# Kernel optimization log

Measured on AMD Instinct MI355X. Metric: run time of the kernel, lower is better.

## Reference

```python
import jax, jax.numpy as jnp
import numpy as np

N_NODES = 50000
N_EDGES = 800000
IN_CH = 64
HID = 64
HID2 = HID // 2  # 32


def _sage_conv(x, src, dst, w_l, w_r, b, n_nodes):
    """PyG SAGEConv (aggr='mean', root_weight=True):
    out = lin_l(mean_{j in N(i)} x_j) + lin_r(x_i), bias in lin_l.
    Messages flow src -> dst (source_to_target)."""
    msg = x[src]  # [E, d] gather of source features
    summed = jax.ops.segment_sum(msg, dst, num_segments=n_nodes)  # [N, d]
    cnt = jax.ops.segment_sum(jnp.ones((src.shape[0],), x.dtype), dst,
                              num_segments=n_nodes)  # [N]
    mean = summed / jnp.maximum(cnt, 1.0)[:, None]
    return mean @ w_l + b + x @ w_r


def setup_inputs() -> dict:
    key = jax.random.key(0)
    ks = jax.random.split(key, 12)
    s = 0.05
    x = jax.random.normal(ks[0], (N_NODES, IN_CH), dtype=jnp.float32)
    edge_index = jax.random.randint(ks[1], (2, N_EDGES), 0, N_NODES, dtype=jnp.int32)
    return {
        "x": x,
        "edge_index": edge_index,
        # SAGEConv layer 1 (in -> hidden)
        "w1_l": jax.random.normal(ks[2], (IN_CH, HID), dtype=jnp.float32) * s,
        "w1_r": jax.random.normal(ks[3], (IN_CH, HID), dtype=jnp.float32) * s,
        "b1": jnp.zeros((HID,), jnp.float32),
        # SAGEConv layer 2 (hidden -> hidden//2)
        "w2_l": jax.random.normal(ks[4], (HID, HID2), dtype=jnp.float32) * s,
        "w2_r": jax.random.normal(ks[5], (HID, HID2), dtype=jnp.float32) * s,
        "b2": jnp.zeros((HID2,), jnp.float32),
        # classifier MLP: Linear(32,16) -> ReLU -> Linear(16,2)
        "wc1": jax.random.normal(ks[6], (HID2, 16), dtype=jnp.float32) * s,
        "bc1": jnp.zeros((16,), jnp.float32),
        "wc2": jax.random.normal(ks[7], (16, 2), dtype=jnp.float32) * s,
        "bc2": jnp.zeros((2,), jnp.float32),
    }


def reference(x, edge_index, w1_l, w1_r, b1, w2_l, w2_r, b2, wc1, bc1, wc2, bc2):
    src, dst = edge_index[0], edge_index[1]
    n = x.shape[0]
    # Dropout is identity in eval / deterministic reference.
    h = jax.nn.relu(_sage_conv(x, src, dst, w1_l, w1_r, b1, n))
    h = jax.nn.relu(_sage_conv(h, src, dst, w2_l, w2_r, b2, n))
    h = jax.nn.relu(h @ wc1 + bc1)
    out = h @ wc2 + bc2  # [N, 2]
    return out
```

## Files before the change

kernel.cpp:

```cpp
#include <hip/hip_runtime.h>
#include <hip/hip_fp16.h>

#define N_NODES 50000
#define N_EDGES 800000
#define NBINS   391
#define CAP     4096
#define EPB     4096
#define NBLK_E  ((N_EDGES + EPB - 1) / EPB)
#define NTILE   391
#define LSTRIDE 129

__global__ __launch_bounds__(512) void k_binA_pre1(
        const int* __restrict__ src, const int* __restrict__ dst,
        int* __restrict__ bincur, int* __restrict__ binned,
        const float* __restrict__ x,
        const float* __restrict__ wl, const float* __restrict__ wr,
        const float* __restrict__ b,
        __half* __restrict__ ph, float* __restrict__ q) {
    __shared__ float smem[64 * LSTRIDE];
    int t = threadIdx.x;
    int bb = blockIdx.x;
    if (bb < NBLK_E) {
        int* cnt  = (int*)smem;
        int* sc   = cnt + 392;
        int* lpos = sc + 512;
        int* base = lpos + 392;
        int* stage = base + 392;
        unsigned short* sbin = (unsigned short*)(stage + EPB);
        int blkbase = bb * EPB;
        int nE = min(EPB, N_EDGES - blkbase);
        for (int i = t; i < NBINS; i += 512) cnt[i] = 0;
        __syncthreads();
        int sv[8], dv[8];
#pragma unroll
        for (int k = 0; k < 8; ++k) {
            int e = blkbase + t + k * 512;
            if (e < N_EDGES) {
                sv[k] = src[e];
                dv[k] = dst[e];
                atomicAdd(&cnt[dv[k] >> 7], 1);
            } else dv[k] = -1;
        }
        __syncthreads();
        sc[t] = (t < NBINS) ? cnt[t] : 0;
        __syncthreads();
        for (int d = 1; d < 512; d <<= 1) {
            int add = (t >= d) ? sc[t - d] : 0;
            __syncthreads();
            sc[t] += add;
            __syncthreads();
        }
        for (int bi = t; bi < NBINS; bi += 512) {
            int excl = sc[bi] - cnt[bi];
            lpos[bi] = excl;
            sc[bi] = excl;
            if (cnt[bi] > 0) base[bi] = bi * CAP + atomicAdd(&bincur[bi], cnt[bi]);
        }
        __syncthreads();
#pragma unroll
        for (int k = 0; k < 8; ++k) {
            if (dv[k] >= 0) {
                int bi = dv[k] >> 7;
                int p = atomicAdd(&lpos[bi], 1);
                stage[p] = (sv[k] & 0xFFFF) | ((dv[k] & 127) << 16);
                sbin[p] = (unsigned short)bi;
            }
        }
        __syncthreads();
        for (int i = t; i < nE; i += 512) {
            int bi = sbin[i];
            int pos = base[bi] + (i - sc[bi]);
            if (pos < (bi + 1) * CAP) binned[pos] = stage[i];
        }
        return;
    }
    float* sx = smem;
    int g0 = (bb - NBLK_E) * 128;
#pragma unroll
    for (int i = 0; i < 4; ++i) {
        int f = t + i * 512;
        int nd = f >> 4, cq = f & 15;
        int gn = g0 + nd;
        float4 v = (gn < N_NODES) ? ((const float4*)x)[(size_t)gn * 16 + cq]
                                  : make_float4(0.f, 0.f, 0.f, 0.f);
        sx[(cq * 4 + 0) * LSTRIDE + nd] = v.x;
        sx[(cq * 4 + 1) * LSTRIDE + nd] = v.y;
        sx[(cq * 4 + 2) * LSTRIDE + nd] = v.z;
        sx[(cq * 4 + 3) * LSTRIDE + nd] = v.w;
    }
    __syncthreads();
    int role = __builtin_amdgcn_readfirstlane(t >> 7);
    int wsel = role >> 1;
    int c0 = (role & 1) * 32;
    int ln = t & 127;
    int node = g0 + ln;
    const float* __restrict__ wm = wsel ? wr : wl;
    float acc[32];
    if (wsel) {
#pragma unroll
        for (int c = 0; c < 32; ++c) acc[c] = b[c0 + c];
    } else {
#pragma unroll
        for (int c = 0; c < 32; ++c) acc[c] = 0.f;
    }
#pragma unroll
    for (int k = 0; k < 64; ++k) {
        float xk = sx[k * LSTRIDE + ln];
#pragma unroll
        for (int c = 0; c < 32; ++c)
            acc[c] = fmaf(xk, wm[k * 64 + c0 + c], acc[c]);
    }
    if (node >= N_NODES) return;
    if (wsel == 0) {
        alignas(16) __half2 hv[16];
#pragma unroll
        for (int i = 0; i < 16; ++i)
            hv[i] = __floats2half2_rn(acc[2 * i], acc[2 * i + 1]);
        float4* op = (float4*)(ph + (size_t)node * 64 + c0);
#pragma unroll
        for (int i = 0; i < 4; ++i) op[i] = ((float4*)hv)[i];
    } else {
        float4* op = (float4*)(q + (size_t)node * 64 + c0);
#pragma unroll
        for (int i = 0; i < 8; ++i)
            op[i] = make_float4(acc[4 * i], acc[4 * i + 1], acc[4 * i + 2], acc[4 * i + 3]);
    }
}

__device__ __forceinline__ void add8(float2& c0, float2& c1, float2& c2, float2& c3,
                                     float4 rv) {
    const __half2* hp = (const __half2*)&rv;
    float2 f0 = __half22float2(hp[0]), f1 = __half22float2(hp[1]);
    float2 f2 = __half22float2(hp[2]), f3 = __half22float2(hp[3]);
    c0.x += f0.x; c0.y += f0.y; c1.x += f1.x; c1.y += f1.y;
    c2.x += f2.x; c2.y += f2.y; c3.x += f3.x; c3.y += f3.y;
}

#define RED2(v, M0, M1)                                         \
    v.x += __shfl_xor(v.x, M0); v.y += __shfl_xor(v.y, M0);     \
    v.x += __shfl_xor(v.x, M1); v.y += __shfl_xor(v.y, M1);

__global__ __launch_bounds__(1024) void k_sort_agg1_pre2(
        const int* __restrict__ bincur, const int* __restrict__ binned,
        int* __restrict__ off, unsigned short* __restrict__ deg,
        int* __restrict__ esrc,
        const __half* __restrict__ ph, const float* __restrict__ q,
        const float* __restrict__ w2l, const float* __restrict__ w2r,
        const float* __restrict__ b2,
        __half* __restrict__ zh, float* __restrict__ r) {
    __shared__ float poolA[64 * LSTRIDE];
    __shared__ int   sbuf[CAP];
    __shared__ int   loff[128];
    __shared__ int   ldeg[128];
    int t = threadIdx.x;
    int bb = blockIdx.x;
    int n0 = bb << 7;
    int seg0 = bb * CAP;
    int n = min(bincur[bb], CAP);
    int* wbuf = (int*)poolA;
    int* cnt  = wbuf + CAP;
    int* tmp  = cnt + 128;
    int* cur  = tmp + 128;
    if (t < 128) cnt[t] = 0;
    for (int i = t; i < n; i += 1024) wbuf[i] = binned[seg0 + i];
    __syncthreads();
    for (int i = t; i < n; i += 1024) atomicAdd(&cnt[wbuf[i] >> 16], 1);
    __syncthreads();
    int v = (t < 128) ? cnt[t] : 0;
    if (t < 128) tmp[t] = v;
    __syncthreads();
    int val = v;
    for (int d = 1; d < 128; d <<= 1) {
        int add = (t >= d && t < 128) ? tmp[t - d] : 0;
        __syncthreads();
        if (t < 128) { val += add; tmp[t] = val; }
        __syncthreads();
    }
    if (t < 128) {
        int excl = val - v;
        cur[t] = excl;
        loff[t] = excl;
        ldeg[t] = v;
        int node = n0 + t;
        if (node < N_NODES) {
            off[node] = seg0 + excl;
            deg[node] = (unsigned short)v;
        }
    }
    __syncthreads();
    for (int i = t; i < n; i += 1024) {
        int w = wbuf[i];
        int p = atomicAdd(&cur[w >> 16], 1);
        sbuf[p] = w & 0xFFFF;
    }
    __syncthreads();
    for (int i = t; i < n; i += 1024) esrc[seg0 + i] = sbuf[i];
    float* sx = poolA;
    {
        int grp = t >> 3;
        int cg  = t & 7;
        int node = n0 + grp;
        if (node < N_NODES) {
            int s0 = loff[grp];
            int dv = ldeg[grp];
            int s1 = s0 + dv;
            const __half* __restrict__ phc = ph + (cg << 3);
            float2 A0 = make_float2(0.f, 0.f), A1 = A0, A2 = A0, A3 = A0;
            float2 B0 = A0, B1 = A0, B2 = A0, B3 = A0;
            float2 C0 = A0, C1 = A0, C2 = A0, C3 = A0;
            float2 D0 = A0, D1 = A0, D2 = A0, D3 = A0;
            for (int i = s0; i < s1; i += 4) {
                add8(A0, A1, A2, A3,
                     *(const float4*)(phc + (size_t)sbuf[i] * 64));
                if (i + 1 < s1) add8(B0, B1, B2, B3,
                     *(const float4*)(phc + (size_t)sbuf[i + 1] * 64));
                if (i + 2 < s1) add8(C0, C1, C2, C3,
                     *(const float4*)(phc + (size_t)sbuf[i + 2] * 64));
                if (i + 3 < s1) add8(D0, D1, D2, D3,
                     *(const float4*)(phc + (size_t)sbuf[i + 3] * 64));
            }
            A0.x += B0.x + (C0.x + D0.x); A0.y += B0.y + (C0.y + D0.y);
            A1.x += B1.x + (C1.x + D1.x); A1.y += B1.y + (C1.y + D1.y);
            A2.x += B2.x + (C2.x + D2.x); A2.y += B2.y + (C2.y + D2.y);
            A3.x += B3.x + (C3.x + D3.x); A3.y += B3.y + (C3.y + D3.y);
            float inv = 1.0f / fmaxf((float)dv, 1.0f);
            const float4* qp = (const float4*)(q + (size_t)node * 64 + (cg << 3));
            float4 q0 = qp[0], q1 = qp[1];
            float* d = sx + (cg << 3) * LSTRIDE + grp;
            d[0 * LSTRIDE] = fmaxf(fmaf(A0.x, inv, q0.x), 0.f);
            d[1 * LSTRIDE] = fmaxf(fmaf(A0.y, inv, q0.y), 0.f);
            d[2 * LSTRIDE] = fmaxf(fmaf(A1.x, inv, q0.z), 0.f);
            d[3 * LSTRIDE] = fmaxf(fmaf(A1.y, inv, q0.w), 0.f);
            d[4 * LSTRIDE] = fmaxf(fmaf(A2.x, inv, q1.x), 0.f);
            d[5 * LSTRIDE] = fmaxf(fmaf(A2.y, inv, q1.y), 0.f);
            d[6 * LSTRIDE] = fmaxf(fmaf(A3.x, inv, q1.z), 0.f);
            d[7 * LSTRIDE] = fmaxf(fmaf(A3.y, inv, q1.w), 0.f);
        }
    }
    __syncthreads();
    int g = __builtin_amdgcn_readfirstlane(t >> 7);
    int role = g & 1;
    int c0 = (g >> 1) * 8;
    int ln = t & 127;
    int node = n0 + ln;
    const float* __restrict__ wm = role ? w2r : w2l;
    float acc[8];
    if (role) {
#pragma unroll
        for (int c = 0; c < 8; ++c) acc[c] = b2[c0 + c];
    } else {
#pragma unroll
        for (int c = 0; c < 8; ++c) acc[c] = 0.f;
    }
#pragma unroll
    for (int k = 0; k < 64; ++k) {
        float xk = sx[k * LSTRIDE + ln];
#pragma unroll
        for (int c = 0; c < 8; ++c)
            acc[c] = fmaf(xk, wm[k * 32 + c0 + c], acc[c]);
    }
    if (node >= N_NODES) return;
    if (role == 0) {
        alignas(16) __half2 hv[4];
#pragma unroll
        for (int i = 0; i < 4; ++i)
            hv[i] = __floats2half2_rn(acc[2 * i], acc[2 * i + 1]);
        *(float4*)(zh + (size_t)node * 32 + c0) = *(float4*)hv;
    } else {
        float4* op = (float4*)(r + (size_t)node * 32 + c0);
        op[0] = make_float4(acc[0], acc[1], acc[2], acc[3]);
        op[1] = make_float4(acc[4], acc[5], acc[6], acc[7]);
    }
}

__global__ __launch_bounds__(256) void k_agg2cls(const int* __restrict__ off,
                                                 const unsigned short* __restrict__ deg,
                                                 const int* __restrict__ esrc,
                                                 const __half* __restrict__ zh,
                                                 const float* __restrict__ r,
                                                 const float* __restrict__ wc1,
                                                 const float* __restrict__ bc1,
                                                 const float* __restrict__ wc2,
                                                 const float* __restrict__ bc2,
                                                 float* __restrict__ out) {
    __shared__ float sh2[16 * 33];
    __shared__ float sh3[16 * 17];
    __shared__ float swc1[512];
    __shared__ float sbc1[16];
    __shared__ float swc2[32];
    __shared__ float sbc2[2];
    int t = threadIdx.x;
    swc1[t] = wc1[t];
    swc1[t + 256] = wc1[t + 256];
    if (t < 16) sbc1[t] = bc1[t];
    if (t < 32) swc2[t] = wc2[t];
    if (t < 2)  sbc2[t] = bc2[t];

    int lane = t & 63;
    int l16 = lane & 15;
    int nl = (t >> 4) & 15;
    int node = blockIdx.x * 16 + nl;
    int eg = l16 >> 2;
    int cg = l16 & 3;
    int s0 = off[node];
    int dv = deg[node];
    int s1 = s0 + dv;
    float2 A0 = make_float2(0.f, 0.f), A1 = A0, A2 = A0, A3 = A0;
    float2 B0 = A0, B1 = A0, B2 = A0, B3 = A0;
    for (int i = s0; i < s1; i += 8) {
        int i0 = i + eg, i1 = i + 4 + eg;
        if (i0 < s1) add8(A0, A1, A2, A3,
            *(const float4*)(zh + (size_t)esrc[i0] * 32 + (cg << 3)));
        if (i1 < s1) add8(B0, B1, B2, B3,
            *(const float4*)(zh + (size_t)esrc[i1] * 32 + (cg << 3)));
    }
    A0.x += B0.x; A0.y += B0.y; A1.x += B1.x; A1.y += B1.y;
    A2.x += B2.x; A2.y += B2.y; A3.x += B3.x; A3.y += B3.y;
    RED2(A0, 4, 8); RED2(A1, 4, 8); RED2(A2, 4, 8); RED2(A3, 4, 8);
    if (eg == 0) {
        float inv = 1.0f / fmaxf((float)dv, 1.0f);
        const float4* rp = (const float4*)(r + (size_t)node * 32 + (cg << 3));
        float4 r0 = rp[0], r1 = rp[1];
        float* d = sh2 + nl * 33 + (cg << 3);
        d[0] = fmaxf(fmaf(A0.x, inv, r0.x), 0.f);
        d[1] = fmaxf(fmaf(A0.y, inv, r0.y), 0.f);
        d[2] = fmaxf(fmaf(A1.x, inv, r0.z), 0.f);
        d[3] = fmaxf(fmaf(A1.y, inv, r0.w), 0.f);
        d[4] = fmaxf(fmaf(A2.x, inv, r1.x), 0.f);
        d[5] = fmaxf(fmaf(A2.y, inv, r1.y), 0.f);
        d[6] = fmaxf(fmaf(A3.x, inv, r1.z), 0.f);
        d[7] = fmaxf(fmaf(A3.y, inv, r1.w), 0.f);
    }
    __syncthreads();
    int n = t >> 4, j = t & 15;
    float acc1 = sbc1[j];
#pragma unroll
    for (int k = 0; k < 32; ++k)
        acc1 = fmaf(sh2[n * 33 + k], swc1[k * 16 + j], acc1);
    sh3[n * 17 + j] = fmaxf(acc1, 0.f);
    __syncthreads();
    if (t < 16) {
        int nn = t;
        float o0 = sbc2[0], o1 = sbc2[1];
#pragma unroll
        for (int k = 0; k < 16; ++k) {
            float h3k = sh3[nn * 17 + k];
            o0 = fmaf(h3k, swc2[k * 2 + 0], o0);
            o1 = fmaf(h3k, swc2[k * 2 + 1], o1);
        }
        int gnode = blockIdx.x * 16 + nn;
        *(float2*)(out + (size_t)gnode * 2) = make_float2(o0, o1);
    }
}

extern "C" void kernel_launch(void* const* d_in, const int* in_sizes, int n_in,
                              void* d_out, int out_size, void* d_ws, size_t ws_size,
                              hipStream_t stream) {
    const float* x   = (const float*)d_in[0];
    const int*   ei  = (const int*)d_in[1];
    const int*   src = ei;
    const int*   dst = ei + N_EDGES;
    const float* w1l = (const float*)d_in[2];
    const float* w1r = (const float*)d_in[3];
    const float* b1  = (const float*)d_in[4];
    const float* w2l = (const float*)d_in[5];
    const float* w2r = (const float*)d_in[6];
    const float* b2  = (const float*)d_in[7];
    const float* wc1 = (const float*)d_in[8];
    const float* bc1 = (const float*)d_in[9];
    const float* wc2 = (const float*)d_in[10];
    const float* bc2 = (const float*)d_in[11];
    float* out = (float*)d_out;

    int*   wi     = (int*)d_ws;
    int*   bincur = wi;
    int*   binned = wi + 400;
    int*   esrc   = binned + (size_t)NBINS * CAP;
    int*   off    = esrc + (size_t)NBINS * CAP;
    unsigned short* deg = (unsigned short*)(off + N_NODES);
    float* q      = (float*)(deg + N_NODES + (N_NODES & 1));
    float* phf    = q + (size_t)64 * N_NODES;
    __half* ph    = (__half*)phf;
    float* zhf    = phf + (size_t)32 * N_NODES;
    __half* zh    = (__half*)zhf;
    float* r      = zhf + (size_t)16 * N_NODES;

    hipMemsetAsync(bincur, 0, 400 * sizeof(int), stream);
    k_binA_pre1<<<NBLK_E + NTILE, 512, 0, stream>>>(src, dst, bincur, binned,
                                                    x, w1l, w1r, b1, ph, q);
    k_sort_agg1_pre2<<<NBINS, 1024, 0, stream>>>(bincur, binned, off, deg, esrc,
                                                 ph, q, w2l, w2r, b2, zh, r);
    k_agg2cls<<<N_NODES / 16, 256, 0, stream>>>(off, deg, esrc, zh, r,
                                                wc1, bc1, wc2, bc2, out);
}
```

Before: 165.8 us.

## Remap layer-2 aggregation to 4 threads per node, 64 nodes per block

```diff
diff --git a/kernel.cpp b/kernel.cpp
--- a/kernel.cpp
+++ b/kernel.cpp
@@ -135,10 +135,6 @@
     c0.x += f0.x; c0.y += f0.y; c1.x += f1.x; c1.y += f1.y;
     c2.x += f2.x; c2.y += f2.y; c3.x += f3.x; c3.y += f3.y;
 }
-
-#define RED2(v, M0, M1)                                         \
-    v.x += __shfl_xor(v.x, M0); v.y += __shfl_xor(v.y, M0);     \
-    v.x += __shfl_xor(v.x, M1); v.y += __shfl_xor(v.y, M1);
 
 __global__ __launch_bounds__(1024) void k_sort_agg1_pre2(
         const int* __restrict__ bincur, const int* __restrict__ binned,
@@ -283,8 +279,8 @@
                                                  const float* __restrict__ wc2,
                                                  const float* __restrict__ bc2,
                                                  float* __restrict__ out) {
-    __shared__ float sh2[16 * 33];
-    __shared__ float sh3[16 * 17];
+    __shared__ float sh2[64 * 33];
+    __shared__ float sh3[64 * 17];
     __shared__ float swc1[512];
     __shared__ float sbc1[16];
     __shared__ float swc2[32];
@@ -295,61 +291,76 @@
     if (t < 16) sbc1[t] = bc1[t];
     if (t < 32) swc2[t] = wc2[t];
     if (t < 2)  sbc2[t] = bc2[t];
-
-    int lane = t & 63;
-    int l16 = lane & 15;
-    int nl = (t >> 4) & 15;
-    int node = blockIdx.x * 16 + nl;
-    int eg = l16 >> 2;
-    int cg = l16 & 3;
-    int s0 = off[node];
-    int dv = deg[node];
-    int s1 = s0 + dv;
-    float2 A0 = make_float2(0.f, 0.f), A1 = A0, A2 = A0, A3 = A0;
-    float2 B0 = A0, B1 = A0, B2 = A0, B3 = A0;
-    for (int i = s0; i < s1; i += 8) {
-        int i0 = i + eg, i1 = i + 4 + eg;
-        if (i0 < s1) add8(A0, A1, A2, A3,
-            *(const float4*)(zh + (size_t)esrc[i0] * 32 + (cg << 3)));
-        if (i1 < s1) add8(B0, B1, B2, B3,
-            *(const float4*)(zh + (size_t)esrc[i1] * 32 + (cg << 3)));
-    }
-    A0.x += B0.x; A0.y += B0.y; A1.x += B1.x; A1.y += B1.y;
-    A2.x += B2.x; A2.y += B2.y; A3.x += B3.x; A3.y += B3.y;
-    RED2(A0, 4, 8); RED2(A1, 4, 8); RED2(A2, 4, 8); RED2(A3, 4, 8);
-    if (eg == 0) {
-        float inv = 1.0f / fmaxf((float)dv, 1.0f);
-        const float4* rp = (const float4*)(r + (size_t)node * 32 + (cg << 3));
-        float4 r0 = rp[0], r1 = rp[1];
-        float* d = sh2 + nl * 33 + (cg << 3);
-        d[0] = fmaxf(fmaf(A0.x, inv, r0.x), 0.f);
-        d[1] = fmaxf(fmaf(A0.y, inv, r0.y), 0.f);
-        d[2] = fmaxf(fmaf(A1.x, inv, r0.z), 0.f);
-        d[3] = fmaxf(fmaf(A1.y, inv, r0.w), 0.f);
-        d[4] = fmaxf(fmaf(A2.x, inv, r1.x), 0.f);
-        d[5] = fmaxf(fmaf(A2.y, inv, r1.y), 0.f);
-        d[6] = fmaxf(fmaf(A3.x, inv, r1.z), 0.f);
-        d[7] = fmaxf(fmaf(A3.y, inv, r1.w), 0.f);
-    }
-    __syncthreads();
-    int n = t >> 4, j = t & 15;
-    float acc1 = sbc1[j];
-#pragma unroll
-    for (int k = 0; k < 32; ++k)
-        acc1 = fmaf(sh2[n * 33 + k], swc1[k * 16 + j], acc1);
-    sh3[n * 17 + j] = fmaxf(acc1, 0.f);
-    __syncthreads();
-    if (t < 16) {
-        int nn = t;
-        float o0 = sbc2[0], o1 = sbc2[1];
-#pragma unroll
-        for (int k = 0; k < 16; ++k) {
-            float h3k = sh3[nn * 17 + k];
-            o0 = fmaf(h3k, swc2[k * 2 + 0], o0);
-            o1 = fmaf(h3k, swc2[k * 2 + 1], o1);
-        }
-        int gnode = blockIdx.x * 16 + nn;
-        *(float2*)(out + (size_t)gnode * 2) = make_float2(o0, o1);
+    __syncthreads();
+
+    int n0 = blockIdx.x << 6;
+    {
+        int nd = t >> 2;
+        int cg = t & 3;
+        int node = n0 + nd;
+        if (node < N_NODES) {
+            int s0 = off[node];
+            int dv = deg[node];
+            int s1 = s0 + dv;
+            const __half* __restrict__ zhc = zh + (cg << 3);
+            float2 A0 = make_float2(0.f, 0.f), A1 = A0, A2 = A0, A3 = A0;
+            float2 B0 = A0, B1 = A0, B2 = A0, B3 = A0;
+            float2 C0 = A0, C1 = A0, C2 = A0, C3 = A0;
+            float2 D0 = A0, D1 = A0, D2 = A0, D3 = A0;
+            for (int i = s0; i < s1; i += 4) {
+                add8(A0, A1, A2, A3,
+                     *(const float4*)(zhc + (size_t)esrc[i] * 32));
+                if (i + 1 < s1) add8(B0, B1, B2, B3,
+                     *(const float4*)(zhc + (size_t)esrc[i + 1] * 32));
+                if (i + 2 < s1) add8(C0, C1, C2, C3,
+                     *(const float4*)(zhc + (size_t)esrc[i + 2] * 32));
+                if (i + 3 < s1) add8(D0, D1, D2, D3,
+                     *(const float4*)(zhc + (size_t)esrc[i + 3] * 32));
+            }
+            A0.x += B0.x + (C0.x + D0.x); A0.y += B0.y + (C0.y + D0.y);
+            A1.x += B1.x + (C1.x + D1.x); A1.y += B1.y + (C1.y + D1.y);
+            A2.x += B2.x + (C2.x + D2.x); A2.y += B2.y + (C2.y + D2.y);
+            A3.x += B3.x + (C3.x + D3.x); A3.y += B3.y + (C3.y + D3.y);
+            float inv = 1.0f / fmaxf((float)dv, 1.0f);
+            const float4* rp = (const float4*)(r + (size_t)node * 32 + (cg << 3));
+            float4 r0 = rp[0], r1 = rp[1];
+            float* d = sh2 + nd * 33 + (cg << 3);
+            d[0] = fmaxf(fmaf(A0.x, inv, r0.x), 0.f);
+            d[1] = fmaxf(fmaf(A0.y, inv, r0.y), 0.f);
+            d[2] = fmaxf(fmaf(A1.x, inv, r0.z), 0.f);
+            d[3] = fmaxf(fmaf(A1.y, inv, r0.w), 0.f);
+            d[4] = fmaxf(fmaf(A2.x, inv, r1.x), 0.f);
+            d[5] = fmaxf(fmaf(A2.y, inv, r1.y), 0.f);
+            d[6] = fmaxf(fmaf(A3.x, inv, r1.z), 0.f);
+            d[7] = fmaxf(fmaf(A3.y, inv, r1.w), 0.f);
+        }
+    }
+    __syncthreads();
+    {
+        int j = t & 15;
+#pragma unroll
+        for (int p = 0; p < 4; ++p) {
+            int nd = (t >> 4) + p * 16;
+            float acc1 = sbc1[j];
+#pragma unroll
+            for (int k = 0; k < 32; ++k)
+                acc1 = fmaf(sh2[nd * 33 + k], swc1[k * 16 + j], acc1);
+            sh3[nd * 17 + j] = fmaxf(acc1, 0.f);
+        }
+    }
+    __syncthreads();
+    if (t < 64) {
+        int node = n0 + t;
+        if (node < N_NODES) {
+            float o0 = sbc2[0], o1 = sbc2[1];
+#pragma unroll
+            for (int k = 0; k < 16; ++k) {
+                float h3k = sh3[t * 17 + k];
+                o0 = fmaf(h3k, swc2[k * 2 + 0], o0);
+                o1 = fmaf(h3k, swc2[k * 2 + 1], o1);
+            }
+            *(float2*)(out + (size_t)node * 2) = make_float2(o0, o1);
+        }
     }
 }
 
@@ -390,6 +401,6 @@
                                                     x, w1l, w1r, b1, ph, q);
     k_sort_agg1_pre2<<<NBINS, 1024, 0, stream>>>(bincur, binned, off, deg, esrc,
                                                  ph, q, w2l, w2r, b2, zh, r);
-    k_agg2cls<<<N_NODES / 16, 256, 0, stream>>>(off, deg, esrc, zh, r,
-                                                wc1, bc1, wc2, bc2, out);
+    k_agg2cls<<<(N_NODES + 63) / 64, 256, 0, stream>>>(off, deg, esrc, zh, r,
+                                                       wc1, bc1, wc2, bc2, out);
 }
```

New measurement: 168.8 us. About the same (+1.8%).
